# Optimization experiments

Measured on AMD Instinct MI355X. Metric: run time of the kernel, lower is better.

The kernel has to match this reference:

```python
import jax, jax.numpy as jnp
import numpy as np

# Standard SMPL kinematic tree (child -> parent); root's entry unused.
PARENTS = np.array([0, 0, 0, 0, 1, 2, 3, 4, 5, 6, 7, 8, 9, 9, 9, 12, 13, 14, 16, 17, 18, 19, 20, 21], dtype=np.int32)
N_JOINTS = 24


def _rodrigues(r):
    # r: [..., 3] axis-angle -> [..., 3, 3] rotation matrices.
    # Original adds N(0,1e-8) noise to avoid div-by-zero; we use a deterministic eps.
    theta = jnp.linalg.norm(r, axis=-1, keepdims=True) + 1e-8
    rh = r / theta
    cos = jnp.cos(theta)[..., None]
    sin = jnp.sin(theta)[..., None]
    z = jnp.zeros_like(rh[..., 0])
    K = jnp.stack([z, -rh[..., 2], rh[..., 1],
                   rh[..., 2], z, -rh[..., 0],
                   -rh[..., 1], rh[..., 0], z], axis=-1).reshape(r.shape[:-1] + (3, 3))
    outer = rh[..., :, None] * rh[..., None, :]
    eye = jnp.eye(3, dtype=r.dtype)
    return cos * eye + (1.0 - cos) * outer + sin * K


def setup_inputs() -> dict:
    key = jax.random.key(0)
    ks = jax.random.split(key, 7)
    N, V, J, B = 512, 6890, 24, 10
    beta = jax.random.normal(ks[0], (N, B), dtype=jnp.float32)
    pose = jax.random.normal(ks[1], (N, J * 3), dtype=jnp.float32)
    v_template = jax.random.normal(ks[2], (V, 3), dtype=jnp.float32)
    shapedirs = jax.random.normal(ks[3], (V, 3, B), dtype=jnp.float32) * 0.03
    posedirs = jax.random.normal(ks[4], (V, 3, (J - 1) * 9), dtype=jnp.float32) * 0.01
    J_regressor = jax.random.uniform(ks[5], (J, V), dtype=jnp.float32)
    J_regressor = J_regressor / jnp.sum(J_regressor, axis=1, keepdims=True)  # NonNegUnitSum(axis=1)
    weights = jax.random.uniform(ks[6], (V, J), dtype=jnp.float32)
    weights = weights / jnp.sum(weights, axis=1, keepdims=True)  # NonNegUnitSum(axis=1)
    return {"beta": beta, "pose": pose, "v_template": v_template, "shapedirs": shapedirs,
            "posedirs": posedirs, "J_regressor": J_regressor, "weights": weights}


def reference(beta, pose, v_template, shapedirs, posedirs, J_regressor, weights):
    N = beta.shape[0]
    dt = beta.dtype
    # Shape blendshapes: [N,V,3]
    v_shaped = jnp.einsum('nb,vcb->nvc', beta, shapedirs) + v_template
    # Joint locations: [N,J,3]
    J_loc = jnp.einsum('jv,nvc->njc', J_regressor, v_shaped)
    # Per-joint rotations: [N,24,3,3]
    R = _rodrigues(pose.reshape(N, N_JOINTS, 3))
    # Pose blendshapes
    lrotmin = (R[:, 1:] - jnp.eye(3, dtype=dt)).reshape(N, (N_JOINTS - 1) * 9)
    v_posed = v_shaped + jnp.einsum('np,vcp->nvc', lrotmin, posedirs)
    # Kinematic chain of 4x4 transforms
    bottom = jnp.broadcast_to(jnp.array([0.0, 0.0, 0.0, 1.0], dtype=dt), (N, 1, 4))

    def make_T(Rm, t):  # [N,3,3], [N,3] -> [N,4,4]
        return jnp.concatenate([jnp.concatenate([Rm, t[..., None]], axis=-1), bottom], axis=-2)

    G = [make_T(R[:, 0], J_loc[:, 0])]
    for i in range(1, N_JOINTS):
        p = int(PARENTS[i])
        G.append(jnp.matmul(G[p], make_T(R[:, i], J_loc[:, i] - J_loc[:, p])))
    G = jnp.stack(G, axis=1)  # [N,24,4,4]
    # Remove rest-pose joint translation: G[...,:,3] -= G @ [J,0]
    Jh = jnp.concatenate([J_loc, jnp.zeros_like(J_loc[..., :1])], axis=-1)  # [N,24,4]
    RJ = jnp.einsum('njab,njb->nja', G, Jh)
    G = G - jnp.pad(RJ[..., None], ((0, 0), (0, 0), (0, 0), (3, 0)))
    # Linear blend skinning: per-vertex blended transform [N,V,4,4]
    T = jnp.einsum('njab,vj->nvab', G, weights)
    vh = jnp.concatenate([v_posed, jnp.ones_like(v_posed[..., :1])], axis=-1)  # [N,V,4]
    v = jnp.einsum('nvab,nvb->nva', T, vh)
    return v[..., :3]
```

## Files before the change

### kernel.cpp

```cpp
#include <hip/hip_runtime.h>

#define V_CNT 6890
#define N_B 512
#define NP 207
#define KPAD 224
#define RTOT 20670
#define RPAD 20736
#define PREP_BLKS 2268
#define JS1_BLKS 192
#define W_BLKS 27

typedef unsigned short ushort_t;
typedef __attribute__((ext_vector_type(4))) float f32x4;
typedef __attribute__((ext_vector_type(8))) short s16x8;
typedef __attribute__((ext_vector_type(2))) float f32x2;

#define O_PART 0u
#define O_G2   65536u
#define O_A    655360u
#define O_W    917504u
#define O_B    1441792u

__device__ __constant__ int PAR[24] = {0,0,0,0,1,2,3,4,5,6,7,8,9,9,9,12,13,14,16,17,18,19,20,21};
__device__ __constant__ int LVL[36] = {
    1, 2, 3,-1,   4, 5, 6,-1,   7, 8, 9,-1,
   10,11,12,13,  14,-1,-1,-1,  15,16,17,-1,
   18,19,-1,-1,  20,21,-1,-1,  22,23,-1,-1};

__device__ __forceinline__ ushort_t f2bf(float f) {
    union { float f; unsigned u; } x; x.f = f;
    unsigned u = x.u + 0x7fffu + ((x.u >> 16) & 1u);
    return (ushort_t)(u >> 16);
}
__device__ __forceinline__ float bf2f(ushort_t h) {
    union { unsigned u; float f; } x; x.u = ((unsigned)h) << 16;
    return x.f;
}

__global__ __launch_bounds__(256) void k_pre(const float* __restrict__ pdirs,
                                             const float* __restrict__ sdirs,
                                             const float* __restrict__ vtemp,
                                             const float* __restrict__ jreg,
                                             const float* __restrict__ wts,
                                             ushort_t* __restrict__ Bswz,
                                             float* __restrict__ part,
                                             ushort_t* __restrict__ Wp) {
    int b = blockIdx.x;
    int tid = threadIdx.x;
    if (b < PREP_BLKS) {
        int g = b * 256 + tid;
        int rtile = g / 448;
        int rem = g - rtile * 448;
        int kc = rem >> 6;
        int lane = rem & 63;
        int quad = lane >> 4, lm = lane & 15;
        int r = rtile * 16 + lm;
        int k0 = kc * 32 + quad * 8;
        s16x8 pk;
        if (r < RTOT) {
            const float* pr = pdirs + (size_t)r * NP;
            const float* sr = sdirs + (size_t)r * 10;
#pragma unroll
            for (int i = 0; i < 8; i++) {
                int k = k0 + i;
                float v = 0.f;
                if (k < NP) v = pr[k];
                else if (k < 217) v = sr[k - NP];
                pk[i] = (short)f2bf(v);
            }
        } else {
#pragma unroll
            for (int i = 0; i < 8; i++) pk[i] = 0;
        }
        *(s16x8*)(Bswz + (size_t)g * 8) = pk;
    } else if (b < PREP_BLKS + JS1_BLKS) {
        int b2 = b - PREP_BLKS;
        int ch = b2 & 7;
        int j = b2 >> 3;
        int v0 = ch * 862;
        int vend = v0 + 862; if (vend > V_CNT) vend = V_CNT;
        float acc[33];
#pragma unroll
        for (int i = 0; i < 33; i++) acc[i] = 0.f;
        for (int v = v0 + tid; v < vend; v += 256) {
            float r = jreg[j * V_CNT + v];
            const float* sd = sdirs + v * 30;
#pragma unroll
            for (int i = 0; i < 30; i++) acc[i] += r * sd[i];
            acc[30] += r * vtemp[v * 3 + 0];
            acc[31] += r * vtemp[v * 3 + 1];
            acc[32] += r * vtemp[v * 3 + 2];
        }
#pragma unroll
        for (int off = 32; off > 0; off >>= 1) {
#pragma unroll
            for (int i = 0; i < 33; i++) acc[i] += __shfl_down(acc[i], off);
        }
        __shared__ float red[4][33];
        int w = tid >> 6, lane = tid & 63;
        if (lane == 0) {
#pragma unroll
            for (int i = 0; i < 33; i++) red[w][i] = acc[i];
        }
        __syncthreads();
        if (tid < 33) {
            float s = red[0][tid] + red[1][tid] + red[2][tid] + red[3][tid];
            part[b2 * 33 + tid] = s;
        }
    } else {
        int v = (b - PREP_BLKS - JS1_BLKS) * 256 + tid;
        ushort_t o[32];
        if (v < V_CNT) {
            const float* wr = wts + v * 24;
#pragma unroll
            for (int j = 0; j < 24; j++) o[j] = f2bf(wr[j]);
        } else {
#pragma unroll
            for (int j = 0; j < 24; j++) o[j] = 0;
        }
#pragma unroll
        for (int j = 24; j < 32; j++) o[j] = 0;
#pragma unroll
        for (int q = 0; q < 4; q++)
            *(s16x8*)(Wp + (size_t)v * 32 + q * 8) = *(s16x8*)&o[q * 8];
    }
}

__global__ __launch_bounds__(128) void k_chain(const float* __restrict__ beta,
                                               const float* __restrict__ pose,
                                               const float* __restrict__ part,
                                               ushort_t* __restrict__ G2,
                                               ushort_t* __restrict__ Aswz) {
    __shared__ float JSl[720];
    __shared__ float JTl[72];
    __shared__ float Rl[2][24][9];
    __shared__ float Jl[2][24][3];
    __shared__ float Tm[2][24][16];
    __shared__ float G[2][24][16];
    __shared__ float Gp[2][24][12];
    int tid = threadIdx.x;

    for (int t = tid; t < 792; t += 128) {
        int j = t / 33, i = t - j * 33;
        float s = 0.f;
#pragma unroll
        for (int c = 0; c < 8; c++) s += part[(j * 8 + c) * 33 + i];
        if (i < 30) JSl[j * 30 + i] = s;
        else        JTl[j * 3 + (i - 30)] = s;
    }
    __syncthreads();

    int sub = tid >> 6, lane = tid & 63;
    int n = blockIdx.x * 2 + sub;

    if (lane < 24) {
        int t = lane;
        float x = pose[n * 72 + t * 3 + 0];
        float y = pose[n * 72 + t * 3 + 1];
        float z = pose[n * 72 + t * 3 + 2];
        float th = sqrtf(x * x + y * y + z * z) + 1e-8f;
        float inv = 1.f / th;
        float rx = x * inv, ry = y * inv, rz = z * inv;
        float c = cosf(th), s = sinf(th), omc = 1.f - c;
        Rl[sub][t][0] = c + omc * rx * rx;
        Rl[sub][t][1] = omc * rx * ry - s * rz;
        Rl[sub][t][2] = omc * rx * rz + s * ry;
        Rl[sub][t][3] = omc * ry * rx + s * rz;
        Rl[sub][t][4] = c + omc * ry * ry;
        Rl[sub][t][5] = omc * ry * rz - s * rx;
        Rl[sub][t][6] = omc * rz * rx - s * ry;
        Rl[sub][t][7] = omc * rz * ry + s * rx;
        Rl[sub][t][8] = c + omc * rz * rz;
#pragma unroll
        for (int cc = 0; cc < 3; cc++) {
            float a = JTl[t * 3 + cc];
#pragma unroll
            for (int b = 0; b < 10; b++) a += beta[n * 10 + b] * JSl[(t * 3 + cc) * 10 + b];
            Jl[sub][t][cc] = a;
        }
    }
    __syncthreads();
    if (lane < 24) {
        int t = lane;
        int p = PAR[t];
        float tx, ty, tz;
        if (t == 0) { tx = Jl[sub][0][0]; ty = Jl[sub][0][1]; tz = Jl[sub][0][2]; }
        else { tx = Jl[sub][t][0] - Jl[sub][p][0]; ty = Jl[sub][t][1] - Jl[sub][p][1]; tz = Jl[sub][t][2] - Jl[sub][p][2]; }
        Tm[sub][t][0] = Rl[sub][t][0]; Tm[sub][t][1] = Rl[sub][t][1]; Tm[sub][t][2]  = Rl[sub][t][2]; Tm[sub][t][3]  = tx;
        Tm[sub][t][4] = Rl[sub][t][3]; Tm[sub][t][5] = Rl[sub][t][4]; Tm[sub][t][6]  = Rl[sub][t][5]; Tm[sub][t][7]  = ty;
        Tm[sub][t][8] = Rl[sub][t][6]; Tm[sub][t][9] = Rl[sub][t][7]; Tm[sub][t][10] = Rl[sub][t][8]; Tm[sub][t][11] = tz;
        Tm[sub][t][12] = 0.f; Tm[sub][t][13] = 0.f; Tm[sub][t][14] = 0.f; Tm[sub][t][15] = 1.f;
    }
    __syncthreads();
    if (lane < 16) G[sub][0][lane] = Tm[sub][0][lane];
    __syncthreads();
#pragma unroll
    for (int p9 = 0; p9 < 9; p9++) {
        int slot = lane >> 4, el = lane & 15;
        int j = LVL[p9 * 4 + slot];
        if (j >= 0) {
            int par = PAR[j];
            int a = el >> 2, bb = el & 3;
            float s = G[sub][par][a * 4 + 0] * Tm[sub][j][0 * 4 + bb]
                    + G[sub][par][a * 4 + 1] * Tm[sub][j][1 * 4 + bb]
                    + G[sub][par][a * 4 + 2] * Tm[sub][j][2 * 4 + bb]
                    + G[sub][par][a * 4 + 3] * Tm[sub][j][3 * 4 + bb];
            G[sub][j][el] = s;
        }
        __syncthreads();
    }
    if (lane < 24) {
        int t = lane;
        float jx = Jl[sub][t][0], jy = Jl[sub][t][1], jz = Jl[sub][t][2];
#pragma unroll
        for (int a = 0; a < 3; a++) {
            float g0 = G[sub][t][a * 4 + 0], g1 = G[sub][t][a * 4 + 1];
            float g2 = G[sub][t][a * 4 + 2], g3 = G[sub][t][a * 4 + 3];
            Gp[sub][t][a * 4 + 0] = g0;
            Gp[sub][t][a * 4 + 1] = g1;
            Gp[sub][t][a * 4 + 2] = g2;
            Gp[sub][t][a * 4 + 3] = g3 - (g0 * jx + g1 * jy + g2 * jz);
        }
    }
    __syncthreads();
    {
        int quad = lane >> 4, lm = lane & 15;
        s16x8 pk;
#pragma unroll
        for (int jj = 0; jj < 8; jj++) {
            int joint = quad * 8 + jj;
            float val = (joint < 24 && lm < 12) ? Gp[sub][joint][lm] : 0.f;
            pk[jj] = (short)f2bf(val);
        }
        *(s16x8*)(G2 + (size_t)n * 512 + lane * 8) = pk;
    }
    if (lane < 28) {
        int kc = lane >> 2, quad2 = lane & 3;
        s16x8 pk;
#pragma unroll
        for (int j = 0; j < 8; j++) {
            int k = kc * 32 + quad2 * 8 + j;
            float val;
            if (k < NP) {
                int jo = 1 + k / 9;
                int e = k - (jo - 1) * 9;
                float d = (e == 0 || e == 4 || e == 8) ? 1.f : 0.f;
                val = Rl[sub][jo][e] - d;
            } else if (k < 217) {
                val = beta[n * 10 + (k - NP)];
            } else val = 0.f;
            pk[j] = (short)f2bf(val);
        }
        *(s16x8*)(Aswz + (((size_t)(n >> 4) * 7 + kc) * 64 + (quad2 * 16 + (n & 15))) * 8) = pk;
    }
}

__global__ __launch_bounds__(256) void k_fused(const ushort_t* __restrict__ Aswz,
                                               const ushort_t* __restrict__ Bswz,
                                               const ushort_t* __restrict__ Wp,
                                               const ushort_t* __restrict__ G2,
                                               const float* __restrict__ vtemp,
                                               float* __restrict__ out) {
    __shared__ ushort_t vp[4][96][34];
    __shared__ float Tl[4][2][32][19];
    __shared__ float ost[4][2][96];
    int tid = threadIdx.x, w = tid >> 6, lane = tid & 63;
    int quad = lane >> 4, lm = lane & 15;
    int rh = w & 1, nh = w >> 1;
    int n_w = blockIdx.y * 64 + nh * 32;
    int vs_w = blockIdx.x * 64 + rh * 32;
    int rtile0 = blockIdx.x * 12 + rh * 6;
    int ntile0 = blockIdx.y * 4 + nh * 2;

    f32x4 acc[2][6];
#pragma unroll
    for (int a = 0; a < 2; a++)
#pragma unroll
        for (int b = 0; b < 6; b++) acc[a][b] = (f32x4)0.f;

    s16x8 af[2][2], bf[2][6];
#pragma unroll
    for (int mt = 0; mt < 2; mt++)
        af[0][mt] = *(const s16x8*)(Aswz + ((size_t)(ntile0 + mt) * 7 + 0) * 512 + lane * 8);
#pragma unroll
    for (int rt = 0; rt < 6; rt++)
        bf[0][rt] = *(const s16x8*)(Bswz + ((size_t)(rtile0 + rt) * 7 + 0) * 512 + lane * 8);
#pragma unroll
    for (int kc = 0; kc < 7; kc++) {
        int cur = kc & 1, nxt = cur ^ 1;
        if (kc < 6) {
#pragma unroll
            for (int mt = 0; mt < 2; mt++)
                af[nxt][mt] = *(const s16x8*)(Aswz + ((size_t)(ntile0 + mt) * 7 + kc + 1) * 512 + lane * 8);
#pragma unroll
            for (int rt = 0; rt < 6; rt++)
                bf[nxt][rt] = *(const s16x8*)(Bswz + ((size_t)(rtile0 + rt) * 7 + kc + 1) * 512 + lane * 8);
        }
#pragma unroll
        for (int mt = 0; mt < 2; mt++)
#pragma unroll
            for (int rt = 0; rt < 6; rt++)
                acc[mt][rt] = __builtin_amdgcn_mfma_f32_16x16x32_bf16(af[cur][mt], bf[cur][rt], acc[mt][rt], 0, 0, 0);
    }

    float vt[6];
#pragma unroll
    for (int rt = 0; rt < 6; rt++) {
        int col = blockIdx.x * 192 + rh * 96 + rt * 16 + lm;
        vt[rt] = (col < RTOT) ? vtemp[col] : 0.f;
    }
#pragma unroll
    for (int mt = 0; mt < 2; mt++) {
#pragma unroll
        for (int rt = 0; rt < 6; rt++) {
            int rl = rt * 16 + lm;
            int nl0 = mt * 16 + quad * 4;
            unsigned d0 = (unsigned)f2bf(acc[mt][rt][0] + vt[rt]) | ((unsigned)f2bf(acc[mt][rt][1] + vt[rt]) << 16);
            unsigned d1 = (unsigned)f2bf(acc[mt][rt][2] + vt[rt]) | ((unsigned)f2bf(acc[mt][rt][3] + vt[rt]) << 16);
            *(unsigned*)&vp[w][rl][nl0]     = d0;
            *(unsigned*)&vp[w][rl][nl0 + 2] = d1;
        }
    }

    s16x8 wf[2];
#pragma unroll
    for (int mt = 0; mt < 2; mt++)
        wf[mt] = *(const s16x8*)(Wp + (size_t)(vs_w + mt * 16 + lm) * 32 + quad * 8);

    int sub = lane >> 5, vl = lane & 31;
    int rem = V_CNT - vs_w;
    int nfl = rem >= 32 ? 96 : rem * 3;
    int nh2 = nfl >> 1;

#pragma unroll 1
    for (int t = 0; t < 16; t++) {
        int na = n_w + 2 * t;
        s16x8 ga = *(const s16x8*)(G2 + (size_t)na * 512 + lane * 8);
        s16x8 gb = *(const s16x8*)(G2 + (size_t)(na + 1) * 512 + lane * 8);
        f32x4 ta[2], tb[2];
#pragma unroll
        for (int mt = 0; mt < 2; mt++) {
            ta[mt] = __builtin_amdgcn_mfma_f32_16x16x32_bf16(wf[mt], ga, (f32x4)0.f, 0, 0, 0);
            tb[mt] = __builtin_amdgcn_mfma_f32_16x16x32_bf16(wf[mt], gb, (f32x4)0.f, 0, 0, 0);
        }
#pragma unroll
        for (int mt = 0; mt < 2; mt++)
#pragma unroll
            for (int i = 0; i < 4; i++) {
                Tl[w][0][mt * 16 + quad * 4 + i][lm] = ta[mt][i];
                Tl[w][1][mt * 16 + quad * 4 + i][lm] = tb[mt][i];
            }
        const float* Tr = &Tl[w][sub][vl][0];
        const ushort_t* pr0 = &vp[w][vl * 3 + 0][2 * t + sub];
        const ushort_t* pr1 = &vp[w][vl * 3 + 1][2 * t + sub];
        const ushort_t* pr2 = &vp[w][vl * 3 + 2][2 * t + sub];
        float p0 = bf2f(*pr0), p1 = bf2f(*pr1), p2 = bf2f(*pr2);
        float o0 = Tr[3]  + Tr[0] * p0 + Tr[1] * p1 + Tr[2]  * p2;
        float o1 = Tr[7]  + Tr[4] * p0 + Tr[5] * p1 + Tr[6]  * p2;
        float o2 = Tr[11] + Tr[8] * p0 + Tr[9] * p1 + Tr[10] * p2;
        ost[w][sub][vl * 3 + 0] = o0;
        ost[w][sub][vl * 3 + 1] = o1;
        ost[w][sub][vl * 3 + 2] = o2;
#pragma unroll
        for (int s2 = 0; s2 < 2; s2++) {
            float* ob = out + ((size_t)(na + s2) * V_CNT + vs_w) * 3;
            if (lane < nh2)
                *(f32x2*)(ob + lane * 2) = *(const f32x2*)&ost[w][s2][lane * 2];
        }
    }
}

extern "C" void kernel_launch(void* const* d_in, const int* in_sizes, int n_in,
                              void* d_out, int out_size, void* d_ws, size_t ws_size,
                              hipStream_t stream) {
    const float* beta  = (const float*)d_in[0];
    const float* pose  = (const float*)d_in[1];
    const float* vtemp = (const float*)d_in[2];
    const float* sdirs = (const float*)d_in[3];
    const float* pdirs = (const float*)d_in[4];
    const float* jreg  = (const float*)d_in[5];
    const float* wts   = (const float*)d_in[6];
    char* ws = (char*)d_ws;
    float*    ws_part = (float*)(ws + O_PART);
    ushort_t* ws_G2   = (ushort_t*)(ws + O_G2);
    ushort_t* ws_A    = (ushort_t*)(ws + O_A);
    ushort_t* ws_W    = (ushort_t*)(ws + O_W);
    ushort_t* ws_B    = (ushort_t*)(ws + O_B);
    float* out = (float*)d_out;

    k_pre<<<dim3(PREP_BLKS + JS1_BLKS + W_BLKS), dim3(256), 0, stream>>>(
        pdirs, sdirs, vtemp, jreg, wts, ws_B, ws_part, ws_W);
    k_chain<<<dim3(N_B / 2), dim3(128), 0, stream>>>(beta, pose, ws_part, ws_G2, ws_A);
    k_fused<<<dim3(108, N_B / 64), dim3(256), 0, stream>>>(ws_A, ws_B, ws_W, ws_G2, vtemp, out);
}
```

Measured before the change: 141.1 us.

## Swap MFMA operands so blended transforms stay in registers, prefetch G2

The skinning MFMA now takes G2 as the A operand and weights as B, so each lane holds one row of the blended 3x4 transform for one vertex. The per-vertex transform is applied directly from registers, dropping the LDS round trips through the Tl and ost staging buffers. The next batch's G2 fragments are prefetched one iteration ahead. Output stores become scalar, strided per-lane writes instead of coalesced float2 writes, and one quarter of the lanes sit idle during the apply step.

```diff
diff --git a/kernel.cpp b/kernel.cpp
--- a/kernel.cpp
+++ b/kernel.cpp
@@ -13,7 +13,7 @@
 typedef unsigned short ushort_t;
 typedef __attribute__((ext_vector_type(4))) float f32x4;
 typedef __attribute__((ext_vector_type(8))) short s16x8;
-typedef __attribute__((ext_vector_type(2))) float f32x2;
+typedef __attribute__((ext_vector_type(4))) short s16x4;
 
 #define O_PART 0u
 #define O_G2   65536u
@@ -261,9 +261,7 @@
                                                const ushort_t* __restrict__ G2,
                                                const float* __restrict__ vtemp,
                                                float* __restrict__ out) {
-    __shared__ ushort_t vp[4][96][34];
-    __shared__ float Tl[4][2][32][19];
-    __shared__ float ost[4][2][96];
+    __shared__ ushort_t vp[4][96][36];
     int tid = threadIdx.x, w = tid >> 6, lane = tid & 63;
     int quad = lane >> 4, lm = lane & 15;
     int rh = w & 1, nh = w >> 1;
@@ -315,10 +313,12 @@
         for (int rt = 0; rt < 6; rt++) {
             int rl = rt * 16 + lm;
             int nl0 = mt * 16 + quad * 4;
-            unsigned d0 = (unsigned)f2bf(acc[mt][rt][0] + vt[rt]) | ((unsigned)f2bf(acc[mt][rt][1] + vt[rt]) << 16);
-            unsigned d1 = (unsigned)f2bf(acc[mt][rt][2] + vt[rt]) | ((unsigned)f2bf(acc[mt][rt][3] + vt[rt]) << 16);
-            *(unsigned*)&vp[w][rl][nl0]     = d0;
-            *(unsigned*)&vp[w][rl][nl0 + 2] = d1;
+            s16x4 pk;
+            pk[0] = (short)f2bf(acc[mt][rt][0] + vt[rt]);
+            pk[1] = (short)f2bf(acc[mt][rt][1] + vt[rt]);
+            pk[2] = (short)f2bf(acc[mt][rt][2] + vt[rt]);
+            pk[3] = (short)f2bf(acc[mt][rt][3] + vt[rt]);
+            *(s16x4*)&vp[w][rl][nl0] = pk;
         }
     }
 
@@ -327,46 +327,42 @@
     for (int mt = 0; mt < 2; mt++)
         wf[mt] = *(const s16x8*)(Wp + (size_t)(vs_w + mt * 16 + lm) * 32 + quad * 8);
 
-    int sub = lane >> 5, vl = lane & 31;
-    int rem = V_CNT - vs_w;
-    int nfl = rem >= 32 ? 96 : rem * 3;
-    int nh2 = nfl >> 1;
-
+    s16x8 ga = *(const s16x8*)(G2 + (size_t)n_w * 512 + lane * 8);
+    s16x8 gb = *(const s16x8*)(G2 + (size_t)(n_w + 1) * 512 + lane * 8);
 #pragma unroll 1
     for (int t = 0; t < 16; t++) {
         int na = n_w + 2 * t;
-        s16x8 ga = *(const s16x8*)(G2 + (size_t)na * 512 + lane * 8);
-        s16x8 gb = *(const s16x8*)(G2 + (size_t)(na + 1) * 512 + lane * 8);
+        s16x8 gan, gbn;
+        if (t < 15) {
+            gan = *(const s16x8*)(G2 + (size_t)(na + 2) * 512 + lane * 8);
+            gbn = *(const s16x8*)(G2 + (size_t)(na + 3) * 512 + lane * 8);
+        }
         f32x4 ta[2], tb[2];
 #pragma unroll
         for (int mt = 0; mt < 2; mt++) {
-            ta[mt] = __builtin_amdgcn_mfma_f32_16x16x32_bf16(wf[mt], ga, (f32x4)0.f, 0, 0, 0);
-            tb[mt] = __builtin_amdgcn_mfma_f32_16x16x32_bf16(wf[mt], gb, (f32x4)0.f, 0, 0, 0);
-        }
-#pragma unroll
-        for (int mt = 0; mt < 2; mt++)
-#pragma unroll
-            for (int i = 0; i < 4; i++) {
-                Tl[w][0][mt * 16 + quad * 4 + i][lm] = ta[mt][i];
-                Tl[w][1][mt * 16 + quad * 4 + i][lm] = tb[mt][i];
+            ta[mt] = __builtin_amdgcn_mfma_f32_16x16x32_bf16(ga, wf[mt], (f32x4)0.f, 0, 0, 0);
+            tb[mt] = __builtin_amdgcn_mfma_f32_16x16x32_bf16(gb, wf[mt], (f32x4)0.f, 0, 0, 0);
+        }
+        if (quad < 3) {
+#pragma unroll
+            for (int mt = 0; mt < 2; mt++) {
+                int v = vs_w + mt * 16 + lm;
+                if (v < V_CNT) {
+                    int vloc = mt * 16 + lm;
+                    unsigned pw0 = *(const unsigned*)&vp[w][vloc * 3 + 0][2 * t];
+                    unsigned pw1 = *(const unsigned*)&vp[w][vloc * 3 + 1][2 * t];
+                    unsigned pw2 = *(const unsigned*)&vp[w][vloc * 3 + 2][2 * t];
+                    float p0a = bf2f((ushort_t)(pw0 & 0xffffu)), p0b = bf2f((ushort_t)(pw0 >> 16));
+                    float p1a = bf2f((ushort_t)(pw1 & 0xffffu)), p1b = bf2f((ushort_t)(pw1 >> 16));
+                    float p2a = bf2f((ushort_t)(pw2 & 0xffffu)), p2b = bf2f((ushort_t)(pw2 >> 16));
+                    float oa = ta[mt][3] + ta[mt][0] * p0a + ta[mt][1] * p1a + ta[mt][2] * p2a;
+                    float ob = tb[mt][3] + tb[mt][0] * p0b + tb[mt][1] * p1b + tb[mt][2] * p2b;
+                    out[((size_t)na * V_CNT + v) * 3 + quad] = oa;
+                    out[((size_t)(na + 1) * V_CNT + v) * 3 + quad] = ob;
+                }
             }
-        const float* Tr = &Tl[w][sub][vl][0];
-        const ushort_t* pr0 = &vp[w][vl * 3 + 0][2 * t + sub];
-        const ushort_t* pr1 = &vp[w][vl * 3 + 1][2 * t + sub];
-        const ushort_t* pr2 = &vp[w][vl * 3 + 2][2 * t + sub];
-        float p0 = bf2f(*pr0), p1 = bf2f(*pr1), p2 = bf2f(*pr2);
-        float o0 = Tr[3]  + Tr[0] * p0 + Tr[1] * p1 + Tr[2]  * p2;
-        float o1 = Tr[7]  + Tr[4] * p0 + Tr[5] * p1 + Tr[6]  * p2;
-        float o2 = Tr[11] + Tr[8] * p0 + Tr[9] * p1 + Tr[10] * p2;
-        ost[w][sub][vl * 3 + 0] = o0;
-        ost[w][sub][vl * 3 + 1] = o1;
-        ost[w][sub][vl * 3 + 2] = o2;
-#pragma unroll
-        for (int s2 = 0; s2 < 2; s2++) {
-            float* ob = out + ((size_t)(na + s2) * V_CNT + vs_w) * 3;
-            if (lane < nh2)
-                *(f32x2*)(ob + lane * 2) = *(const f32x2*)&ost[w][s2][lane * 2];
-        }
+        }
+        ga = gan; gb = gbn;
     }
 }
 
```

New measurement: 138.4 us. No clear change (-1.9%).
